# Kernel tuning notes

Hardware: AMD Instinct MI355X
Metric: run time of the kernel (lower is better)

The kernel has to match this reference:

```python
import jax, jax.numpy as jnp
import numpy as np

B = 131072
K = 64           # vertices per body
P = 4            # extract directions
D = 7 + 3 * K    # config (pos3 + quat4) + flattened vertices


def quat_to_rotmat(q):
    """q: (B,4) as (w,x,y,z) -> (B,3,3) rotation matrices (unit-quaternion formula)."""
    w, x, y, z = q[:, 0], q[:, 1], q[:, 2], q[:, 3]
    two = jnp.asarray(2.0, q.dtype)
    one = jnp.asarray(1.0, q.dtype)
    R = jnp.stack([
        one - two * (y * y + z * z), two * (x * y - z * w),       two * (x * z + y * w),
        two * (x * y + z * w),       one - two * (x * x + z * z), two * (y * z - x * w),
        two * (x * z - y * w),       two * (y * z + x * w),       one - two * (x * x + y * y),
    ], axis=-1)
    return R.reshape(-1, 3, 3)


def setup_inputs() -> dict:
    key = jax.random.key(0)
    k1, k2 = jax.random.split(key)
    x = jax.random.normal(k1, (B, 1, D), dtype=jnp.float32)
    extract_dirs = jax.random.normal(k2, (P, 3), dtype=jnp.float32)
    return {"x": x, "extract_dirs": extract_dirs}


def reference(x, extract_dirs):
    # x: (B, 1, D).  Original code transposes to (B, D, 1) and loops per sample;
    # here we batch the whole thing.
    xf = x[:, 0, :]                       # (B, D)
    pos = xf[:, 0:3]                      # (B, 3) translation
    quat = xf[:, 3:7]                     # (B, 4) quaternion (w,x,y,z)
    verts = xf[:, 7:].reshape(-1, K, 3)   # (B, K, 3): reshape(k,3) rows = vertices
    R = quat_to_rotmat(quat)              # (B, 3, 3)
    # rotate (R @ v) then translate: world coords of each vertex
    world = jnp.einsum('bij,bkj->bki', R, verts) + pos[:, None, :]  # (B, K, 3)
    # project onto extract directions; torch does ed.bmm(coords) -> (p,k), then
    # transpose(1,2) -> (k,p); cat over batch -> (B, K, P)
    return jnp.einsum('bki,pi->bkp', world, extract_dirs)
```

## Files before the change

kernel.cpp:

```cpp
#include <hip/hip_runtime.h>


constexpr int B = 131072;
constexpr int K = 64;
constexpr int P = 4;
constexpr int D = 7 + 3 * K;

struct F3 { float a, b, c; };

__global__ __launch_bounds__(256) void vde_kernel(const float* __restrict__ x,
                                                  const float* __restrict__ dirs,
                                                  float* __restrict__ out) {
    const int tid  = blockIdx.x * blockDim.x + threadIdx.x;
    const int lane = threadIdx.x & 63;
    const int b    = tid >> 6;

    const int rowoff = __builtin_amdgcn_readfirstlane(b * D);
    const float* row = x + rowoff;

    const float px = row[0], py = row[1], pz = row[2];
    const float qw = row[3], qx = row[4], qy = row[5], qz = row[6];

    const float xx = qx * qx, yy = qy * qy, zz = qz * qz;
    const float xy = qx * qy, xz = qx * qz, yz = qy * qz;
    const float wx = qw * qx, wy = qw * qy, wz = qw * qz;

    const float r00 = 1.0f - 2.0f * (yy + zz);
    const float r01 = 2.0f * (xy - wz);
    const float r02 = 2.0f * (xz + wy);
    const float r10 = 2.0f * (xy + wz);
    const float r11 = 1.0f - 2.0f * (xx + zz);
    const float r12 = 2.0f * (yz - wx);
    const float r20 = 2.0f * (xz - wy);
    const float r21 = 2.0f * (yz + wx);
    const float r22 = 1.0f - 2.0f * (xx + yy);

    const F3 v = *reinterpret_cast<const F3*>(row + 7 + 3 * lane);

    float4 o;
    float* op = &o.x;
#pragma unroll
    for (int p = 0; p < P; ++p) {
        const float d0 = dirs[p * 3 + 0];
        const float d1 = dirs[p * 3 + 1];
        const float d2 = dirs[p * 3 + 2];
        const float m0 = d0 * r00 + d1 * r10 + d2 * r20;
        const float m1 = d0 * r01 + d1 * r11 + d2 * r21;
        const float m2 = d0 * r02 + d1 * r12 + d2 * r22;
        const float c  = d0 * px + d1 * py + d2 * pz;
        op[p] = v.a * m0 + v.b * m1 + v.c * m2 + c;
    }

    *reinterpret_cast<float4*>(out + (size_t)tid * 4) = o;
}

extern "C" void kernel_launch(void* const* d_in, const int* in_sizes, int n_in,
                              void* d_out, int out_size, void* d_ws, size_t ws_size,
                              hipStream_t stream) {
    const float* x    = (const float*)d_in[0];
    const float* dirs = (const float*)d_in[1];
    float* out        = (float*)d_out;

    const int total_threads = B * K;
    const int block = 256;
    const int grid = total_threads / block;
    vde_kernel<<<grid, block, 0, stream>>>(x, dirs, out);
}
```

Baseline: 206.0 us.

## Use grid-stride loop with nontemporal loads and stores, hoist direction loads

```diff
diff --git a/kernel.cpp b/kernel.cpp
--- a/kernel.cpp
+++ b/kernel.cpp
@@ -7,51 +7,66 @@
 constexpr int D = 7 + 3 * K;
 
 struct F3 { float a, b, c; };
+typedef float f32x4 __attribute__((ext_vector_type(4)));
 
 __global__ __launch_bounds__(256) void vde_kernel(const float* __restrict__ x,
                                                   const float* __restrict__ dirs,
                                                   float* __restrict__ out) {
-    const int tid  = blockIdx.x * blockDim.x + threadIdx.x;
-    const int lane = threadIdx.x & 63;
-    const int b    = tid >> 6;
-
-    const int rowoff = __builtin_amdgcn_readfirstlane(b * D);
-    const float* row = x + rowoff;
-
-    const float px = row[0], py = row[1], pz = row[2];
-    const float qw = row[3], qx = row[4], qy = row[5], qz = row[6];
-
-    const float xx = qx * qx, yy = qy * qy, zz = qz * qz;
-    const float xy = qx * qy, xz = qx * qz, yz = qy * qz;
-    const float wx = qw * qx, wy = qw * qy, wz = qw * qz;
-
-    const float r00 = 1.0f - 2.0f * (yy + zz);
-    const float r01 = 2.0f * (xy - wz);
-    const float r02 = 2.0f * (xz + wy);
-    const float r10 = 2.0f * (xy + wz);
-    const float r11 = 1.0f - 2.0f * (xx + zz);
-    const float r12 = 2.0f * (yz - wx);
-    const float r20 = 2.0f * (xz - wy);
-    const float r21 = 2.0f * (yz + wx);
-    const float r22 = 1.0f - 2.0f * (xx + yy);
-
-    const F3 v = *reinterpret_cast<const F3*>(row + 7 + 3 * lane);
-
-    float4 o;
-    float* op = &o.x;
+    float d0v[P], d1v[P], d2v[P];
 #pragma unroll
     for (int p = 0; p < P; ++p) {
-        const float d0 = dirs[p * 3 + 0];
-        const float d1 = dirs[p * 3 + 1];
-        const float d2 = dirs[p * 3 + 2];
-        const float m0 = d0 * r00 + d1 * r10 + d2 * r20;
-        const float m1 = d0 * r01 + d1 * r11 + d2 * r21;
-        const float m2 = d0 * r02 + d1 * r12 + d2 * r22;
-        const float c  = d0 * px + d1 * py + d2 * pz;
-        op[p] = v.a * m0 + v.b * m1 + v.c * m2 + c;
+        d0v[p] = dirs[p * 3 + 0];
+        d1v[p] = dirs[p * 3 + 1];
+        d2v[p] = dirs[p * 3 + 2];
     }
 
-    *reinterpret_cast<float4*>(out + (size_t)tid * 4) = o;
+    const int lane = threadIdx.x & 63;
+    const int nthreads = gridDim.x * blockDim.x;
+    const int total = B * K;
+
+    for (int tid = blockIdx.x * blockDim.x + threadIdx.x; tid < total;
+         tid += nthreads) {
+        const int b = tid >> 6;
+
+        const int rowoff = __builtin_amdgcn_readfirstlane(b * D);
+        const float* row = x + rowoff;
+
+        const float px = row[0], py = row[1], pz = row[2];
+        const float qw = row[3], qx = row[4], qy = row[5], qz = row[6];
+
+        const float xx = qx * qx, yy = qy * qy, zz = qz * qz;
+        const float xy = qx * qy, xz = qx * qz, yz = qy * qz;
+        const float wx = qw * qx, wy = qw * qy, wz = qw * qz;
+
+        const float r00 = 1.0f - 2.0f * (yy + zz);
+        const float r01 = 2.0f * (xy - wz);
+        const float r02 = 2.0f * (xz + wy);
+        const float r10 = 2.0f * (xy + wz);
+        const float r11 = 1.0f - 2.0f * (xx + zz);
+        const float r12 = 2.0f * (yz - wx);
+        const float r20 = 2.0f * (xz - wy);
+        const float r21 = 2.0f * (yz + wx);
+        const float r22 = 1.0f - 2.0f * (xx + yy);
+
+        const F3* vp = reinterpret_cast<const F3*>(row + 7 + 3 * lane);
+        F3 v;
+        v.a = __builtin_nontemporal_load(&vp->a);
+        v.b = __builtin_nontemporal_load(&vp->b);
+        v.c = __builtin_nontemporal_load(&vp->c);
+
+        f32x4 o;
+#pragma unroll
+        for (int p = 0; p < P; ++p) {
+            const float m0 = d0v[p] * r00 + d1v[p] * r10 + d2v[p] * r20;
+            const float m1 = d0v[p] * r01 + d1v[p] * r11 + d2v[p] * r21;
+            const float m2 = d0v[p] * r02 + d1v[p] * r12 + d2v[p] * r22;
+            const float c  = d0v[p] * px + d1v[p] * py + d2v[p] * pz;
+            o[p] = v.a * m0 + v.b * m1 + v.c * m2 + c;
+        }
+
+        f32x4* outp = reinterpret_cast<f32x4*>(out + (size_t)tid * 4);
+        __builtin_nontemporal_store(o, outp);
+    }
 }
 
 extern "C" void kernel_launch(void* const* d_in, const int* in_sizes, int n_in,
@@ -61,8 +76,7 @@
     const float* dirs = (const float*)d_in[1];
     float* out        = (float*)d_out;
 
-    const int total_threads = B * K;
     const int block = 256;
-    const int grid = total_threads / block;
+    const int grid = 2048;
     vde_kernel<<<grid, block, 0, stream>>>(x, dirs, out);
 }
```

Result: slower. 217.3 us (+5.5%).
